# Kernel tuning notes

Measured on AMD Instinct MI355X. Metric: run time of the kernel, lower is better.

Reference implementation:

```python
import jax, jax.numpy as jnp
import numpy as np

B = 524288
NF, NH1, NH21, NH22, NCLS = 5, 128, 32, 32, 1


def setup_inputs() -> dict:
    key = jax.random.key(0)
    ks = jax.random.split(key, 12)
    s = 0.05
    return {
        "x": jax.random.normal(ks[0], (B, NF), dtype=jnp.float32),
        "mean": jnp.zeros((NF,), dtype=jnp.float32),
        "std": jnp.ones((NF,), dtype=jnp.float32),
        "W1": jax.random.normal(ks[1], (NH1, NF), dtype=jnp.float32) * s,
        "b1": jax.random.normal(ks[2], (NH1,), dtype=jnp.float32) * s,
        "W21": jax.random.normal(ks[3], (NH21, NH1), dtype=jnp.float32) * s,
        "b21": jax.random.normal(ks[4], (NH21,), dtype=jnp.float32) * s,
        "W22": jax.random.normal(ks[5], (NH22, NH1), dtype=jnp.float32) * s,
        "b22": jax.random.normal(ks[6], (NH22,), dtype=jnp.float32) * s,
        "W31": jax.random.normal(ks[7], (NCLS, NH21), dtype=jnp.float32) * s,
        "b31": jax.random.normal(ks[8], (NCLS,), dtype=jnp.float32) * s,
        "W32": jax.random.normal(ks[9], (NCLS, NH22), dtype=jnp.float32) * s,
        "b32": jax.random.normal(ks[10], (NCLS,), dtype=jnp.float32) * s,
    }


def reference(x, mean, std, W1, b1, W21, b21, W22, b22, W31, b31, W32, b32):
    # de-normalized state used to build the CBF inequality
    x0 = x * std + mean  # [B, 5]
    h1 = jax.nn.relu(x @ W1.T + b1)         # [B, 128]  (bn=False path)
    x21 = jax.nn.relu(h1 @ W21.T + b21)     # [B, 32]
    x22 = jax.nn.relu(h1 @ W22.T + b22)     # [B, 32]
    x31 = x21 @ W31.T + b31                 # [B, 1]  QP linear term p
    x32 = 4.0 * jax.nn.sigmoid(x22 @ W32.T + b32)  # [B, 1]  learned penalty
    # h for the single inequality 1.8*u <= h
    h = (x0[:, 1] - x0[:, 3])[:, None] + x32 * (x0[:, 0] - x0[:, 2] - 1.8 * x0[:, 3])[:, None]
    # Closed-form 1-D QP: min 0.5 u^2 + x31*u  s.t. 1.8 u <= h
    u_unc = -x31
    u = jnp.where(1.8 * u_unc <= h, u_unc, h / 1.8)  # [B, 1]
    return u
```

## Files before the change

kernel.cpp:

```cpp
#include <hip/hip_runtime.h>
#include <math.h>

typedef __attribute__((ext_vector_type(8))) short bf16x8;
typedef __attribute__((ext_vector_type(4))) float f32x4;
typedef __attribute__((ext_vector_type(4))) unsigned int u32x4;

#define BLK 256


__device__ __forceinline__ unsigned int rne_bf16_bits(float w) {
    unsigned int u = __builtin_bit_cast(unsigned int, w);
    u += 0x7fffu + ((u >> 16) & 1u);
    return u >> 16;
}
__device__ __forceinline__ float bf16_to_f32(unsigned int bits) {
    return __builtin_bit_cast(float, bits << 16);
}

__global__ void setup_kernel(const float* __restrict__ W1, const float* __restrict__ b1,
                             const float* __restrict__ W21, const float* __restrict__ W22,
                             unsigned short* __restrict__ w1f, unsigned short* __restrict__ frg)
{
    int t = blockIdx.x * blockDim.x + threadIdx.x;
    {
        int e = t;
        int nt = e >> 9, l = (e >> 3) & 63, j = e & 7;
        int n = nt * 16 + (l & 15), q = l >> 4;
        unsigned short v = 0;
        if (q == 0) {
            if (j < 5)       v = (unsigned short)rne_bf16_bits(W1[n * 5 + j]);
            else if (j == 5) v = (unsigned short)rne_bf16_bits(b1[n]);
        } else if (q == 1) {
            if (j < 5) {
                unsigned int h = rne_bf16_bits(W1[n * 5 + j]);
                v = (unsigned short)rne_bf16_bits(W1[n * 5 + j] - bf16_to_f32(h));
            } else if (j == 5) {
                unsigned int h = rne_bf16_bits(b1[n]);
                v = (unsigned short)rne_bf16_bits(b1[n] - bf16_to_f32(h));
            }
        } else if (q == 2) {
            if (j < 5)       v = (unsigned short)rne_bf16_bits(W1[n * 5 + j]);
        }
        w1f[e] = v;
    }
    for (int e = t; e < 16 * 64 * 8; e += 4096) {
        int F = e >> 9, l = (e >> 3) & 63, j = e & 7;
        int mat = F >> 3, nt2 = (F >> 2) & 1, kt = F & 3;
        int n2 = nt2 * 16 + (l & 15), q = l >> 4;
        int ks = 16 * (2 * kt + (j >> 2)) + 4 * q + (j & 3);
        const float* W = mat ? W22 : W21;
        frg[e] = (unsigned short)rne_bf16_bits(W[n2 * 128 + ks]);
    }
}

__global__ __launch_bounds__(BLK, 4) void barriernet_kernel(
    const float* __restrict__ x,
    const float* __restrict__ mean, const float* __restrict__ stdv,
    const float* __restrict__ b21, const float* __restrict__ b22,
    const float* __restrict__ W31, const float* __restrict__ b31,
    const float* __restrict__ W32, const float* __restrict__ b32,
    const u32x4* __restrict__ w1fg, const u32x4* __restrict__ frg,
    float* __restrict__ out, int zero)
{
    __shared__ u32x4 ldsF[1024];

    const int tid = threadIdx.x;
    #pragma unroll
    for (int i = 0; i < 4; ++i) ldsF[tid + i * BLK] = frg[tid + i * BLK];

    const int lane = tid & 63;
    const int wave = tid >> 6;
    const int m    = lane & 15;
    const int q    = lane >> 4;

    u32x4 w1f[8];
    #pragma unroll
    for (int nt = 0; nt < 8; ++nt) w1f[nt] = w1fg[nt * 64 + lane];

    float sm_s[5], sm_m[5];
    #pragma unroll
    for (int f = 0; f < 5; ++f) { sm_s[f] = stdv[f]; sm_m[f] = mean[f]; }
    const float b31s = b31[0], b32s = b32[0];

    __syncthreads();

    const size_t wrow0 = (size_t)blockIdx.x * 512 + wave * 128;

    float4 xc4; float xc1;
    {
        const float* p = x + (wrow0 + m) * 5;
        xc4 = *(const float4*)p; xc1 = p[4];
    }

    #pragma unroll 1
    for (int it = 0; it < 8; ++it) {
        const int itn = (it < 7) ? it + 1 : 7;
        const float* pn = x + (wrow0 + itn * 16 + m) * 5;
        float4 xn4 = *(const float4*)pn;
        float  xn1 = pn[4];

        const float xf[5] = { xc4.x, xc4.y, xc4.z, xc4.w, xc1 };

        unsigned int hb[5], lb[5];
        #pragma unroll
        for (int f = 0; f < 5; ++f) {
            hb[f] = rne_bf16_bits(xf[f]);
            lb[f] = rne_bf16_bits(xf[f] - bf16_to_f32(hb[f]));
        }
        const unsigned int xh01 = hb[0] | (hb[1] << 16);
        const unsigned int xh23 = hb[2] | (hb[3] << 16);
        const unsigned int xh4b = hb[4] | (0x3F80u << 16);
        const unsigned int xl01 = lb[0] | (lb[1] << 16);
        const unsigned int xl23 = lb[2] | (lb[3] << 16);
        const unsigned int xl4  = lb[4];
        const bool ql2 = (q < 2), q2 = (q == 2);
        u32x4 xd;
        xd[0] = ql2 ? xh01 : (q2 ? xl01 : 0u);
        xd[1] = ql2 ? xh23 : (q2 ? xl23 : 0u);
        xd[2] = ql2 ? xh4b : (q2 ? xl4  : 0u);
        xd[3] = 0u;
        const bf16x8 xb = __builtin_bit_cast(bf16x8, xd);

        unsigned int au[4][4];
        #pragma unroll
        for (int kt = 0; kt < 4; ++kt) {
            f32x4 z = { 0.0f, 0.0f, 0.0f, 0.0f };
            f32x4 d0 = __builtin_amdgcn_mfma_f32_16x16x32_bf16(
                __builtin_bit_cast(bf16x8, w1f[2 * kt]),     xb, z, 0, 0, 0);
            f32x4 d1 = __builtin_amdgcn_mfma_f32_16x16x32_bf16(
                __builtin_bit_cast(bf16x8, w1f[2 * kt + 1]), xb, z, 0, 0, 0);
            au[kt][0] = rne_bf16_bits(fmaxf(d0[0], 0.0f)) | (rne_bf16_bits(fmaxf(d0[1], 0.0f)) << 16);
            au[kt][1] = rne_bf16_bits(fmaxf(d0[2], 0.0f)) | (rne_bf16_bits(fmaxf(d0[3], 0.0f)) << 16);
            au[kt][2] = rne_bf16_bits(fmaxf(d1[0], 0.0f)) | (rne_bf16_bits(fmaxf(d1[1], 0.0f)) << 16);
            au[kt][3] = rne_bf16_bits(fmaxf(d1[2], 0.0f)) | (rne_bf16_bits(fmaxf(d1[3], 0.0f)) << 16);
        }

        const float* bz21 = b21 + it * zero;
        const float* bz22 = b22 + it * zero;
        const float* wz31 = W31 + it * zero;
        const float* wz32 = W32 + it * zero;
        f32x4 acc[4];
        acc[0] = *(const f32x4*)(bz21 + q * 4);
        acc[1] = *(const f32x4*)(bz21 + 16 + q * 4);
        acc[2] = *(const f32x4*)(bz22 + q * 4);
        acc[3] = *(const f32x4*)(bz22 + 16 + q * 4);

        const int fz = it * zero;
        #pragma unroll
        for (int kt = 0; kt < 4; ++kt) {
            u32x4 t4 = { au[kt][0], au[kt][1], au[kt][2], au[kt][3] };
            const bf16x8 a = __builtin_bit_cast(bf16x8, t4);
            #pragma unroll
            for (int c = 0; c < 4; ++c) {
                const int F = (c >> 1) * 8 + (c & 1) * 4 + kt;
                const bf16x8 bw = __builtin_bit_cast(bf16x8, ldsF[F * 64 + lane + fz]);
                acc[c] = __builtin_amdgcn_mfma_f32_16x16x32_bf16(bw, a, acc[c], 0, 0, 0);
            }
        }

        const f32x4 w31a = *(const f32x4*)(wz31 + q * 4);
        const f32x4 w31b = *(const f32x4*)(wz31 + 16 + q * 4);
        const f32x4 w32a = *(const f32x4*)(wz32 + q * 4);
        const f32x4 w32b = *(const f32x4*)(wz32 + 16 + q * 4);
        float s31 = 0.0f, s32 = 0.0f;
        #pragma unroll
        for (int r = 0; r < 4; ++r) {
            s31 = fmaf(fmaxf(acc[0][r], 0.0f), w31a[r], s31);
            s31 = fmaf(fmaxf(acc[1][r], 0.0f), w31b[r], s31);
            s32 = fmaf(fmaxf(acc[2][r], 0.0f), w32a[r], s32);
            s32 = fmaf(fmaxf(acc[3][r], 0.0f), w32b[r], s32);
        }
        s31 += __shfl_xor(s31, 16);
        s31 += __shfl_xor(s31, 32);
        s32 += __shfl_xor(s32, 16);
        s32 += __shfl_xor(s32, 32);

        const float x31 = s31 + b31s;
        const float z   = s32 + b32s;
        const float x32 = 4.0f / (1.0f + __expf(-z));
        float x0[5];
        #pragma unroll
        for (int f = 0; f < 5; ++f) x0[f] = fmaf(xf[f], sm_s[f], sm_m[f]);
        const float h_ineq = (x0[1] - x0[3]) + x32 * (x0[0] - x0[2] - 1.8f * x0[3]);
        const float u_unc  = -x31;
        const float u      = (1.8f * u_unc <= h_ineq) ? u_unc : (h_ineq / 1.8f);
        if (lane < 16)
            out[wrow0 + it * 16 + lane] = u;

        xc4 = xn4; xc1 = xn1;
    }
}

extern "C" void kernel_launch(void* const* d_in, const int* in_sizes, int n_in,
                              void* d_out, int out_size, void* d_ws, size_t ws_size,
                              hipStream_t stream) {
    const float* x    = (const float*)d_in[0];
    const float* mean = (const float*)d_in[1];
    const float* stdv = (const float*)d_in[2];
    const float* W1   = (const float*)d_in[3];
    const float* b1   = (const float*)d_in[4];
    const float* W21  = (const float*)d_in[5];
    const float* b21  = (const float*)d_in[6];
    const float* W22  = (const float*)d_in[7];
    const float* b22  = (const float*)d_in[8];
    const float* W31  = (const float*)d_in[9];
    const float* b31  = (const float*)d_in[10];
    const float* W32  = (const float*)d_in[11];
    const float* b32  = (const float*)d_in[12];
    float* out = (float*)d_out;

    unsigned short* w1f = (unsigned short*)d_ws;
    unsigned short* frg = (unsigned short*)((char*)d_ws + 8192);

    setup_kernel<<<16, 256, 0, stream>>>(W1, b1, W21, W22, w1f, frg);

    barriernet_kernel<<<1024, BLK, 0, stream>>>(
        x, mean, stdv, b21, b22, W31, b31, W32, b32,
        (const u32x4*)w1f, (const u32x4*)frg, out, 0);
}
```

Baseline: 110.1 us.

## Process two 16-row tiles per iteration and hoist per-layer weights into registers

The main loop now handles two 16-row tiles per iteration, halving the trip count. Each LDS fragment load of the second-layer weights is reused across both tiles, and independent MFMA chains are interleaved. Biases and head weights are loaded once before the loop instead of every iteration. Bf16 packing now uses the HIP packed conversion intrinsic, and launch bounds drop from 4 to 3 blocks per SIMD to allow the higher register use, at the cost of occupancy.

```diff
diff --git a/kernel.cpp b/kernel.cpp
--- a/kernel.cpp
+++ b/kernel.cpp
@@ -1,5 +1,7 @@
 #include <hip/hip_runtime.h>
+#include <hip/hip_bf16.h>
 #include <math.h>
+#include <string.h>
 
 typedef __attribute__((ext_vector_type(8))) short bf16x8;
 typedef __attribute__((ext_vector_type(4))) float f32x4;
@@ -15,6 +17,11 @@
 }
 __device__ __forceinline__ float bf16_to_f32(unsigned int bits) {
     return __builtin_bit_cast(float, bits << 16);
+}
+__device__ __forceinline__ unsigned int pk_bf16(float lo, float hi) {
+    __hip_bfloat162 bp = __float22bfloat162_rn(make_float2(lo, hi));
+    unsigned int r; memcpy(&r, &bp, 4);
+    return r;
 }
 
 __global__ void setup_kernel(const float* __restrict__ W1, const float* __restrict__ b1,
@@ -53,7 +60,7 @@
     }
 }
 
-__global__ __launch_bounds__(BLK, 4) void barriernet_kernel(
+__global__ __launch_bounds__(BLK, 3) void barriernet_kernel(
     const float* __restrict__ x,
     const float* __restrict__ mean, const float* __restrict__ stdv,
     const float* __restrict__ b21, const float* __restrict__ b22,
@@ -77,6 +84,16 @@
     #pragma unroll
     for (int nt = 0; nt < 8; ++nt) w1f[nt] = w1fg[nt * 64 + lane];
 
+    f32x4 bac[4], whv[4];
+    bac[0] = *(const f32x4*)(b21 + q * 4);
+    bac[1] = *(const f32x4*)(b21 + 16 + q * 4);
+    bac[2] = *(const f32x4*)(b22 + q * 4);
+    bac[3] = *(const f32x4*)(b22 + 16 + q * 4);
+    whv[0] = *(const f32x4*)(W31 + q * 4);
+    whv[1] = *(const f32x4*)(W31 + 16 + q * 4);
+    whv[2] = *(const f32x4*)(W32 + q * 4);
+    whv[3] = *(const f32x4*)(W32 + 16 + q * 4);
+
     float sm_s[5], sm_m[5];
     #pragma unroll
     for (int f = 0; f < 5; ++f) { sm_s[f] = stdv[f]; sm_m[f] = mean[f]; }
@@ -86,108 +103,121 @@
 
     const size_t wrow0 = (size_t)blockIdx.x * 512 + wave * 128;
 
-    float4 xc4; float xc1;
-    {
-        const float* p = x + (wrow0 + m) * 5;
-        xc4 = *(const float4*)p; xc1 = p[4];
+    float4 xc4[2]; float xc1[2];
+    #pragma unroll
+    for (int T = 0; T < 2; ++T) {
+        const float* p = x + (wrow0 + T * 16 + m) * 5;
+        xc4[T] = *(const float4*)p; xc1[T] = p[4];
     }
 
     #pragma unroll 1
-    for (int it = 0; it < 8; ++it) {
-        const int itn = (it < 7) ? it + 1 : 7;
-        const float* pn = x + (wrow0 + itn * 16 + m) * 5;
-        float4 xn4 = *(const float4*)pn;
-        float  xn1 = pn[4];
-
-        const float xf[5] = { xc4.x, xc4.y, xc4.z, xc4.w, xc1 };
-
-        unsigned int hb[5], lb[5];
-        #pragma unroll
-        for (int f = 0; f < 5; ++f) {
-            hb[f] = rne_bf16_bits(xf[f]);
-            lb[f] = rne_bf16_bits(xf[f] - bf16_to_f32(hb[f]));
-        }
-        const unsigned int xh01 = hb[0] | (hb[1] << 16);
-        const unsigned int xh23 = hb[2] | (hb[3] << 16);
-        const unsigned int xh4b = hb[4] | (0x3F80u << 16);
-        const unsigned int xl01 = lb[0] | (lb[1] << 16);
-        const unsigned int xl23 = lb[2] | (lb[3] << 16);
-        const unsigned int xl4  = lb[4];
-        const bool ql2 = (q < 2), q2 = (q == 2);
-        u32x4 xd;
-        xd[0] = ql2 ? xh01 : (q2 ? xl01 : 0u);
-        xd[1] = ql2 ? xh23 : (q2 ? xl23 : 0u);
-        xd[2] = ql2 ? xh4b : (q2 ? xl4  : 0u);
-        xd[3] = 0u;
-        const bf16x8 xb = __builtin_bit_cast(bf16x8, xd);
-
-        unsigned int au[4][4];
+    for (int it = 0; it < 4; ++it) {
+        const int itn = (it < 3) ? it + 1 : 3;
+        float4 xn4[2]; float xn1[2];
+        #pragma unroll
+        for (int T = 0; T < 2; ++T) {
+            const float* pn = x + (wrow0 + itn * 32 + T * 16 + m) * 5;
+            xn4[T] = *(const float4*)pn; xn1[T] = pn[4];
+        }
+
+        float xf[2][5];
+        #pragma unroll
+        for (int T = 0; T < 2; ++T) {
+            xf[T][0] = xc4[T].x; xf[T][1] = xc4[T].y; xf[T][2] = xc4[T].z;
+            xf[T][3] = xc4[T].w; xf[T][4] = xc1[T];
+        }
+
+        unsigned int au[2][4][4];
+        #pragma unroll
+        for (int T = 0; T < 2; ++T) {
+            unsigned int hb[5], lb[5];
+            #pragma unroll
+            for (int f = 0; f < 5; ++f) {
+                hb[f] = rne_bf16_bits(xf[T][f]);
+                lb[f] = rne_bf16_bits(xf[T][f] - bf16_to_f32(hb[f]));
+            }
+            const unsigned int xh01 = hb[0] | (hb[1] << 16);
+            const unsigned int xh23 = hb[2] | (hb[3] << 16);
+            const unsigned int xh4b = hb[4] | (0x3F80u << 16);
+            const unsigned int xl01 = lb[0] | (lb[1] << 16);
+            const unsigned int xl23 = lb[2] | (lb[3] << 16);
+            const unsigned int xl4  = lb[4];
+            const bool ql2 = (q < 2), q2 = (q == 2);
+            u32x4 xd;
+            xd[0] = ql2 ? xh01 : (q2 ? xl01 : 0u);
+            xd[1] = ql2 ? xh23 : (q2 ? xl23 : 0u);
+            xd[2] = ql2 ? xh4b : (q2 ? xl4  : 0u);
+            xd[3] = 0u;
+            const bf16x8 xb = __builtin_bit_cast(bf16x8, xd);
+
+            #pragma unroll
+            for (int kt = 0; kt < 4; ++kt) {
+                f32x4 z = { 0.0f, 0.0f, 0.0f, 0.0f };
+                f32x4 d0 = __builtin_amdgcn_mfma_f32_16x16x32_bf16(
+                    __builtin_bit_cast(bf16x8, w1f[2 * kt]),     xb, z, 0, 0, 0);
+                f32x4 d1 = __builtin_amdgcn_mfma_f32_16x16x32_bf16(
+                    __builtin_bit_cast(bf16x8, w1f[2 * kt + 1]), xb, z, 0, 0, 0);
+                au[T][kt][0] = pk_bf16(fmaxf(d0[0], 0.0f), fmaxf(d0[1], 0.0f));
+                au[T][kt][1] = pk_bf16(fmaxf(d0[2], 0.0f), fmaxf(d0[3], 0.0f));
+                au[T][kt][2] = pk_bf16(fmaxf(d1[0], 0.0f), fmaxf(d1[1], 0.0f));
+                au[T][kt][3] = pk_bf16(fmaxf(d1[2], 0.0f), fmaxf(d1[3], 0.0f));
+            }
+        }
+
+        f32x4 acc[2][4];
+        #pragma unroll
+        for (int T = 0; T < 2; ++T)
+            #pragma unroll
+            for (int c = 0; c < 4; ++c) acc[T][c] = bac[c];
+        const int fz = it * zero;
         #pragma unroll
         for (int kt = 0; kt < 4; ++kt) {
-            f32x4 z = { 0.0f, 0.0f, 0.0f, 0.0f };
-            f32x4 d0 = __builtin_amdgcn_mfma_f32_16x16x32_bf16(
-                __builtin_bit_cast(bf16x8, w1f[2 * kt]),     xb, z, 0, 0, 0);
-            f32x4 d1 = __builtin_amdgcn_mfma_f32_16x16x32_bf16(
-                __builtin_bit_cast(bf16x8, w1f[2 * kt + 1]), xb, z, 0, 0, 0);
-            au[kt][0] = rne_bf16_bits(fmaxf(d0[0], 0.0f)) | (rne_bf16_bits(fmaxf(d0[1], 0.0f)) << 16);
-            au[kt][1] = rne_bf16_bits(fmaxf(d0[2], 0.0f)) | (rne_bf16_bits(fmaxf(d0[3], 0.0f)) << 16);
-            au[kt][2] = rne_bf16_bits(fmaxf(d1[0], 0.0f)) | (rne_bf16_bits(fmaxf(d1[1], 0.0f)) << 16);
-            au[kt][3] = rne_bf16_bits(fmaxf(d1[2], 0.0f)) | (rne_bf16_bits(fmaxf(d1[3], 0.0f)) << 16);
-        }
-
-        const float* bz21 = b21 + it * zero;
-        const float* bz22 = b22 + it * zero;
-        const float* wz31 = W31 + it * zero;
-        const float* wz32 = W32 + it * zero;
-        f32x4 acc[4];
-        acc[0] = *(const f32x4*)(bz21 + q * 4);
-        acc[1] = *(const f32x4*)(bz21 + 16 + q * 4);
-        acc[2] = *(const f32x4*)(bz22 + q * 4);
-        acc[3] = *(const f32x4*)(bz22 + 16 + q * 4);
-
-        const int fz = it * zero;
-        #pragma unroll
-        for (int kt = 0; kt < 4; ++kt) {
-            u32x4 t4 = { au[kt][0], au[kt][1], au[kt][2], au[kt][3] };
-            const bf16x8 a = __builtin_bit_cast(bf16x8, t4);
+            bf16x8 bw[4];
             #pragma unroll
             for (int c = 0; c < 4; ++c) {
                 const int F = (c >> 1) * 8 + (c & 1) * 4 + kt;
-                const bf16x8 bw = __builtin_bit_cast(bf16x8, ldsF[F * 64 + lane + fz]);
-                acc[c] = __builtin_amdgcn_mfma_f32_16x16x32_bf16(bw, a, acc[c], 0, 0, 0);
-            }
-        }
-
-        const f32x4 w31a = *(const f32x4*)(wz31 + q * 4);
-        const f32x4 w31b = *(const f32x4*)(wz31 + 16 + q * 4);
-        const f32x4 w32a = *(const f32x4*)(wz32 + q * 4);
-        const f32x4 w32b = *(const f32x4*)(wz32 + 16 + q * 4);
-        float s31 = 0.0f, s32 = 0.0f;
-        #pragma unroll
-        for (int r = 0; r < 4; ++r) {
-            s31 = fmaf(fmaxf(acc[0][r], 0.0f), w31a[r], s31);
-            s31 = fmaf(fmaxf(acc[1][r], 0.0f), w31b[r], s31);
-            s32 = fmaf(fmaxf(acc[2][r], 0.0f), w32a[r], s32);
-            s32 = fmaf(fmaxf(acc[3][r], 0.0f), w32b[r], s32);
-        }
-        s31 += __shfl_xor(s31, 16);
-        s31 += __shfl_xor(s31, 32);
-        s32 += __shfl_xor(s32, 16);
-        s32 += __shfl_xor(s32, 32);
-
-        const float x31 = s31 + b31s;
-        const float z   = s32 + b32s;
-        const float x32 = 4.0f / (1.0f + __expf(-z));
-        float x0[5];
-        #pragma unroll
-        for (int f = 0; f < 5; ++f) x0[f] = fmaf(xf[f], sm_s[f], sm_m[f]);
-        const float h_ineq = (x0[1] - x0[3]) + x32 * (x0[0] - x0[2] - 1.8f * x0[3]);
-        const float u_unc  = -x31;
-        const float u      = (1.8f * u_unc <= h_ineq) ? u_unc : (h_ineq / 1.8f);
-        if (lane < 16)
-            out[wrow0 + it * 16 + lane] = u;
-
-        xc4 = xn4; xc1 = xn1;
+                bw[c] = __builtin_bit_cast(bf16x8, ldsF[F * 64 + lane + fz]);
+            }
+            #pragma unroll
+            for (int T = 0; T < 2; ++T) {
+                u32x4 t4 = { au[T][kt][0], au[T][kt][1], au[T][kt][2], au[T][kt][3] };
+                const bf16x8 a = __builtin_bit_cast(bf16x8, t4);
+                #pragma unroll
+                for (int c = 0; c < 4; ++c)
+                    acc[T][c] = __builtin_amdgcn_mfma_f32_16x16x32_bf16(bw[c], a, acc[T][c], 0, 0, 0);
+            }
+        }
+
+        #pragma unroll
+        for (int T = 0; T < 2; ++T) {
+            float s31 = 0.0f, s32 = 0.0f;
+            #pragma unroll
+            for (int r = 0; r < 4; ++r) {
+                s31 = fmaf(fmaxf(acc[T][0][r], 0.0f), whv[0][r], s31);
+                s31 = fmaf(fmaxf(acc[T][1][r], 0.0f), whv[1][r], s31);
+                s32 = fmaf(fmaxf(acc[T][2][r], 0.0f), whv[2][r], s32);
+                s32 = fmaf(fmaxf(acc[T][3][r], 0.0f), whv[3][r], s32);
+            }
+            s31 += __shfl_xor(s31, 16);
+            s31 += __shfl_xor(s31, 32);
+            s32 += __shfl_xor(s32, 16);
+            s32 += __shfl_xor(s32, 32);
+
+            const float x31 = s31 + b31s;
+            const float z   = s32 + b32s;
+            const float x32 = 4.0f / (1.0f + __expf(-z));
+            float x0[5];
+            #pragma unroll
+            for (int f = 0; f < 5; ++f) x0[f] = fmaf(xf[T][f], sm_s[f], sm_m[f]);
+            const float h_ineq = (x0[1] - x0[3]) + x32 * (x0[0] - x0[2] - 1.8f * x0[3]);
+            const float u_unc  = -x31;
+            const float u      = (1.8f * u_unc <= h_ineq) ? u_unc : (h_ineq / 1.8f);
+            if (lane < 16)
+                out[wrow0 + it * 32 + T * 16 + lane] = u;
+        }
+
+        #pragma unroll
+        for (int T = 0; T < 2; ++T) { xc4[T] = xn4[T]; xc1[T] = xn1[T]; }
     }
 }
 
```

Result: no change. 108.0 us (-1.9%).

## Switch MLP layers to 32x32x16 MFMA and process 32 rows per wave iteration

Applied to the files above, without the earlier changes.

Replaces the 16x16x32 bf16 MFMA tiles with 32x32x16 tiles for both the first layer and the two hidden heads, so each wave handles 32 batch rows per iteration and 256 rows in total. The weight fragment layouts in the setup kernel are rebuilt to match. It also drops the split-precision handling of x (the separate low-part contribution), packs bf16 with the library conversion, hoists bias and output weights into registers, and halves the grid. This cuts MFMA instruction count, the shuffles and the per-iteration global loads, at the cost of more registers (launch bounds lowered to 2 blocks per SIMD), fewer blocks, and lower input precision in the first layer.

```diff
diff --git a/kernel.cpp b/kernel.cpp
--- a/kernel.cpp
+++ b/kernel.cpp
@@ -1,8 +1,11 @@
 #include <hip/hip_runtime.h>
+#include <hip/hip_bf16.h>
 #include <math.h>
+#include <string.h>
 
 typedef __attribute__((ext_vector_type(8))) short bf16x8;
 typedef __attribute__((ext_vector_type(4))) float f32x4;
+typedef __attribute__((ext_vector_type(16))) float f32x16;
 typedef __attribute__((ext_vector_type(4))) unsigned int u32x4;
 
 #define BLK 256
@@ -15,6 +18,11 @@
 }
 __device__ __forceinline__ float bf16_to_f32(unsigned int bits) {
     return __builtin_bit_cast(float, bits << 16);
+}
+__device__ __forceinline__ unsigned int pk_bf16(float lo, float hi) {
+    __hip_bfloat162 bp = __float22bfloat162_rn(make_float2(lo, hi));
+    unsigned int r; memcpy(&r, &bp, 4);
+    return r;
 }
 
 __global__ void setup_kernel(const float* __restrict__ W1, const float* __restrict__ b1,
@@ -22,38 +30,33 @@
                              unsigned short* __restrict__ w1f, unsigned short* __restrict__ frg)
 {
     int t = blockIdx.x * blockDim.x + threadIdx.x;
-    {
+    if (t < 2048) {
         int e = t;
-        int nt = e >> 9, l = (e >> 3) & 63, j = e & 7;
-        int n = nt * 16 + (l & 15), q = l >> 4;
+        int tt = e >> 9, l = (e >> 3) & 63, j = e & 7;
+        int n = tt * 32 + (l & 31), h = l >> 5;
         unsigned short v = 0;
-        if (q == 0) {
-            if (j < 5)       v = (unsigned short)rne_bf16_bits(W1[n * 5 + j]);
-            else if (j == 5) v = (unsigned short)rne_bf16_bits(b1[n]);
-        } else if (q == 1) {
-            if (j < 5) {
-                unsigned int h = rne_bf16_bits(W1[n * 5 + j]);
-                v = (unsigned short)rne_bf16_bits(W1[n * 5 + j] - bf16_to_f32(h));
-            } else if (j == 5) {
-                unsigned int h = rne_bf16_bits(b1[n]);
-                v = (unsigned short)rne_bf16_bits(b1[n] - bf16_to_f32(h));
-            }
-        } else if (q == 2) {
-            if (j < 5)       v = (unsigned short)rne_bf16_bits(W1[n * 5 + j]);
+        float src = 0.0f; bool have = false;
+        if (j < 5)       { src = W1[n * 5 + j]; have = true; }
+        else if (j == 5) { src = b1[n];         have = true; }
+        if (have) {
+            unsigned int hi = rne_bf16_bits(src);
+            if (h == 0) v = (unsigned short)hi;
+            else        v = (unsigned short)rne_bf16_bits(src - bf16_to_f32(hi));
         }
         w1f[e] = v;
     }
     for (int e = t; e < 16 * 64 * 8; e += 4096) {
         int F = e >> 9, l = (e >> 3) & 63, j = e & 7;
-        int mat = F >> 3, nt2 = (F >> 2) & 1, kt = F & 3;
-        int n2 = nt2 * 16 + (l & 15), q = l >> 4;
-        int ks = 16 * (2 * kt + (j >> 2)) + 4 * q + (j & 3);
+        int mat = F >> 3, kt = F & 7;
+        int tt = kt >> 1, c = kt & 1;
+        int n2 = l & 31, h = l >> 5;
+        int k = 32 * tt + 16 * c + 4 * h + (j & 3) + 8 * (j >> 2);
         const float* W = mat ? W22 : W21;
-        frg[e] = (unsigned short)rne_bf16_bits(W[n2 * 128 + ks]);
-    }
-}
-
-__global__ __launch_bounds__(BLK, 4) void barriernet_kernel(
+        frg[e] = (unsigned short)rne_bf16_bits(W[n2 * 128 + k]);
+    }
+}
+
+__global__ __launch_bounds__(BLK, 2) void barriernet_kernel(
     const float* __restrict__ x,
     const float* __restrict__ mean, const float* __restrict__ stdv,
     const float* __restrict__ b21, const float* __restrict__ b22,
@@ -70,12 +73,21 @@
 
     const int lane = tid & 63;
     const int wave = tid >> 6;
-    const int m    = lane & 15;
-    const int q    = lane >> 4;
-
-    u32x4 w1f[8];
-    #pragma unroll
-    for (int nt = 0; nt < 8; ++nt) w1f[nt] = w1fg[nt * 64 + lane];
+    const int R    = lane & 31;
+    const int h    = lane >> 5;
+
+    u32x4 w1f[4];
+    #pragma unroll
+    for (int t = 0; t < 4; ++t) w1f[t] = w1fg[t * 64 + lane];
+
+    f32x4 bc21[4], bc22[4], wh31[4], wh32[4];
+    #pragma unroll
+    for (int rq = 0; rq < 4; ++rq) {
+        bc21[rq] = *(const f32x4*)(b21 + 8 * rq + 4 * h);
+        bc22[rq] = *(const f32x4*)(b22 + 8 * rq + 4 * h);
+        wh31[rq] = *(const f32x4*)(W31 + 8 * rq + 4 * h);
+        wh32[rq] = *(const f32x4*)(W32 + 8 * rq + 4 * h);
+    }
 
     float sm_s[5], sm_m[5];
     #pragma unroll
@@ -84,95 +96,72 @@
 
     __syncthreads();
 
-    const size_t wrow0 = (size_t)blockIdx.x * 512 + wave * 128;
+    const size_t wrow0 = (size_t)blockIdx.x * 1024 + wave * 256;
 
     float4 xc4; float xc1;
     {
-        const float* p = x + (wrow0 + m) * 5;
+        const float* p = x + (wrow0 + R) * 5;
         xc4 = *(const float4*)p; xc1 = p[4];
     }
 
     #pragma unroll 1
     for (int it = 0; it < 8; ++it) {
         const int itn = (it < 7) ? it + 1 : 7;
-        const float* pn = x + (wrow0 + itn * 16 + m) * 5;
+        const float* pn = x + (wrow0 + itn * 32 + R) * 5;
         float4 xn4 = *(const float4*)pn;
         float  xn1 = pn[4];
 
         const float xf[5] = { xc4.x, xc4.y, xc4.z, xc4.w, xc1 };
 
-        unsigned int hb[5], lb[5];
-        #pragma unroll
-        for (int f = 0; f < 5; ++f) {
-            hb[f] = rne_bf16_bits(xf[f]);
-            lb[f] = rne_bf16_bits(xf[f] - bf16_to_f32(hb[f]));
-        }
-        const unsigned int xh01 = hb[0] | (hb[1] << 16);
-        const unsigned int xh23 = hb[2] | (hb[3] << 16);
-        const unsigned int xh4b = hb[4] | (0x3F80u << 16);
-        const unsigned int xl01 = lb[0] | (lb[1] << 16);
-        const unsigned int xl23 = lb[2] | (lb[3] << 16);
-        const unsigned int xl4  = lb[4];
-        const bool ql2 = (q < 2), q2 = (q == 2);
         u32x4 xd;
-        xd[0] = ql2 ? xh01 : (q2 ? xl01 : 0u);
-        xd[1] = ql2 ? xh23 : (q2 ? xl23 : 0u);
-        xd[2] = ql2 ? xh4b : (q2 ? xl4  : 0u);
+        xd[0] = pk_bf16(xf[0], xf[1]);
+        xd[1] = pk_bf16(xf[2], xf[3]);
+        xd[2] = pk_bf16(xf[4], 1.0f);
         xd[3] = 0u;
         const bf16x8 xb = __builtin_bit_cast(bf16x8, xd);
 
-        unsigned int au[4][4];
-        #pragma unroll
-        for (int kt = 0; kt < 4; ++kt) {
-            f32x4 z = { 0.0f, 0.0f, 0.0f, 0.0f };
-            f32x4 d0 = __builtin_amdgcn_mfma_f32_16x16x32_bf16(
-                __builtin_bit_cast(bf16x8, w1f[2 * kt]),     xb, z, 0, 0, 0);
-            f32x4 d1 = __builtin_amdgcn_mfma_f32_16x16x32_bf16(
-                __builtin_bit_cast(bf16x8, w1f[2 * kt + 1]), xb, z, 0, 0, 0);
-            au[kt][0] = rne_bf16_bits(fmaxf(d0[0], 0.0f)) | (rne_bf16_bits(fmaxf(d0[1], 0.0f)) << 16);
-            au[kt][1] = rne_bf16_bits(fmaxf(d0[2], 0.0f)) | (rne_bf16_bits(fmaxf(d0[3], 0.0f)) << 16);
-            au[kt][2] = rne_bf16_bits(fmaxf(d1[0], 0.0f)) | (rne_bf16_bits(fmaxf(d1[1], 0.0f)) << 16);
-            au[kt][3] = rne_bf16_bits(fmaxf(d1[2], 0.0f)) | (rne_bf16_bits(fmaxf(d1[3], 0.0f)) << 16);
+        unsigned int au[8][4];
+        #pragma unroll
+        for (int t = 0; t < 4; ++t) {
+            f32x16 z = {};
+            f32x16 D = __builtin_amdgcn_mfma_f32_32x32x16_bf16(
+                __builtin_bit_cast(bf16x8, w1f[t]), xb, z, 0, 0, 0);
+            #pragma unroll
+            for (int c = 0; c < 2; ++c)
+                #pragma unroll
+                for (int d = 0; d < 4; ++d)
+                    au[2 * t + c][d] = pk_bf16(fmaxf(D[8 * c + 2 * d],     0.0f),
+                                               fmaxf(D[8 * c + 2 * d + 1], 0.0f));
         }
 
-        const float* bz21 = b21 + it * zero;
-        const float* bz22 = b22 + it * zero;
-        const float* wz31 = W31 + it * zero;
-        const float* wz32 = W32 + it * zero;
-        f32x4 acc[4];
-        acc[0] = *(const f32x4*)(bz21 + q * 4);
-        acc[1] = *(const f32x4*)(bz21 + 16 + q * 4);
-        acc[2] = *(const f32x4*)(bz22 + q * 4);
-        acc[3] = *(const f32x4*)(bz22 + 16 + q * 4);
-
+        f32x16 acc21, acc22;
+        #pragma unroll
+        for (int rq = 0; rq < 4; ++rq)
+            #pragma unroll
+            for (int r = 0; r < 4; ++r) {
+                acc21[rq * 4 + r] = bc21[rq][r];
+                acc22[rq * 4 + r] = bc22[rq][r];
+            }
         const int fz = it * zero;
         #pragma unroll
-        for (int kt = 0; kt < 4; ++kt) {
+        for (int kt = 0; kt < 8; ++kt) {
             u32x4 t4 = { au[kt][0], au[kt][1], au[kt][2], au[kt][3] };
-            const bf16x8 a = __builtin_bit_cast(bf16x8, t4);
+            const bf16x8 b = __builtin_bit_cast(bf16x8, t4);
+            const bf16x8 wa21 = __builtin_bit_cast(bf16x8, ldsF[kt * 64 + lane + fz]);
+            const bf16x8 wa22 = __builtin_bit_cast(bf16x8, ldsF[(8 + kt) * 64 + lane + fz]);
+            acc21 = __builtin_amdgcn_mfma_f32_32x32x16_bf16(wa21, b, acc21, 0, 0, 0);
+            acc22 = __builtin_amdgcn_mfma_f32_32x32x16_bf16(wa22, b, acc22, 0, 0, 0);
+        }
+
+        float s31 = 0.0f, s32 = 0.0f;
+        #pragma unroll
+        for (int rq = 0; rq < 4; ++rq)
             #pragma unroll
-            for (int c = 0; c < 4; ++c) {
-                const int F = (c >> 1) * 8 + (c & 1) * 4 + kt;
-                const bf16x8 bw = __builtin_bit_cast(bf16x8, ldsF[F * 64 + lane + fz]);
-                acc[c] = __builtin_amdgcn_mfma_f32_16x16x32_bf16(bw, a, acc[c], 0, 0, 0);
+            for (int r = 0; r < 4; ++r) {
+                s31 = fmaf(fmaxf(acc21[rq * 4 + r], 0.0f), wh31[rq][r], s31);
+                s32 = fmaf(fmaxf(acc22[rq * 4 + r], 0.0f), wh32[rq][r], s32);
             }
-        }
-
-        const f32x4 w31a = *(const f32x4*)(wz31 + q * 4);
-        const f32x4 w31b = *(const f32x4*)(wz31 + 16 + q * 4);
-        const f32x4 w32a = *(const f32x4*)(wz32 + q * 4);
-        const f32x4 w32b = *(const f32x4*)(wz32 + 16 + q * 4);
-        float s31 = 0.0f, s32 = 0.0f;
-        #pragma unroll
-        for (int r = 0; r < 4; ++r) {
-            s31 = fmaf(fmaxf(acc[0][r], 0.0f), w31a[r], s31);
-            s31 = fmaf(fmaxf(acc[1][r], 0.0f), w31b[r], s31);
-            s32 = fmaf(fmaxf(acc[2][r], 0.0f), w32a[r], s32);
-            s32 = fmaf(fmaxf(acc[3][r], 0.0f), w32b[r], s32);
-        }
-        s31 += __shfl_xor(s31, 16);
         s31 += __shfl_xor(s31, 32);
-        s32 += __shfl_xor(s32, 16);
         s32 += __shfl_xor(s32, 32);
 
         const float x31 = s31 + b31s;
@@ -184,8 +173,8 @@
         const float h_ineq = (x0[1] - x0[3]) + x32 * (x0[0] - x0[2] - 1.8f * x0[3]);
         const float u_unc  = -x31;
         const float u      = (1.8f * u_unc <= h_ineq) ? u_unc : (h_ineq / 1.8f);
-        if (lane < 16)
-            out[wrow0 + it * 16 + lane] = u;
+        if (lane < 32)
+            out[wrow0 + it * 32 + R] = u;
 
         xc4 = xn4; xc1 = xn1;
     }
@@ -210,11 +199,11 @@
     float* out = (float*)d_out;
 
     unsigned short* w1f = (unsigned short*)d_ws;
-    unsigned short* frg = (unsigned short*)((char*)d_ws + 8192);
+    unsigned short* frg = (unsigned short*)((char*)d_ws + 4096);
 
     setup_kernel<<<16, 256, 0, stream>>>(W1, b1, W21, W22, w1f, frg);
 
-    barriernet_kernel<<<1024, BLK, 0, stream>>>(
+    barriernet_kernel<<<512, BLK, 0, stream>>>(
         x, mean, stdv, b21, b22, W31, b31, W32, b32,
         (const u32x4*)w1f, (const u32x4*)frg, out, 0);
 }
```

Result: faster. 103.9 us (-5.6%).
